# Kernel tuning notes

Measured on AMD Instinct MI355X. Metric: run time of the kernel, lower is better.

## Reference

```python
import jax, jax.numpy as jnp
import numpy as np

NUM_LABELS = 64
BATCH = 1024
SEQ_LEN = 512


def setup_inputs() -> dict:
    key = jax.random.key(0)
    k1, k2, k3, k4 = jax.random.split(key, 4)
    emissions = jax.random.normal(k1, (BATCH, SEQ_LEN, NUM_LABELS), dtype=jnp.float32)
    mask = jnp.ones((BATCH, SEQ_LEN), dtype=jnp.int32)
    # params: uniform(-0.1, 0.1) as in nn.init.uniform_
    transitions = jax.random.uniform(k2, (NUM_LABELS, NUM_LABELS), minval=-0.1, maxval=0.1, dtype=jnp.float32)
    start_transitions = jax.random.uniform(k3, (NUM_LABELS,), minval=-0.1, maxval=0.1, dtype=jnp.float32)
    end_transitions = jax.random.uniform(k4, (NUM_LABELS,), minval=-0.1, maxval=0.1, dtype=jnp.float32)
    return {
        "emissions": emissions,
        "mask": mask,
        "transitions": transitions,
        "start_transitions": start_transitions,
        "end_transitions": end_transitions,
    }


def reference(emissions, mask, transitions, start_transitions, end_transitions):
    """CRF forward algorithm (log partition) -> [batch]."""
    # initial alpha: start + emissions at t=0  -> [B, L]
    score0 = start_transitions + emissions[:, 0]

    # scan over time steps 1..S-1
    emit_rest = jnp.swapaxes(emissions[:, 1:], 0, 1)          # [S-1, B, L]
    mask_rest = jnp.swapaxes(mask[:, 1:], 0, 1)               # [S-1, B]

    def step(score, xs):
        emit_t, mask_t = xs                                   # [B, L], [B]
        # [B, L_prev, 1] + [L_prev, L_next] + [B, 1, L_next]
        next_score = jax.nn.logsumexp(
            score[:, :, None] + transitions[None] + emit_t[:, None, :], axis=1
        )                                                     # [B, L]
        score = jnp.where(mask_t[:, None].astype(bool), next_score, score)
        return score, None

    score, _ = jax.lax.scan(step, score0, (emit_rest, mask_rest))
    return jax.nn.logsumexp(score + end_transitions, axis=1)  # [B]
```

## Files before the change

kernel.cpp:

```cpp
#include <hip/hip_runtime.h>

#define NL 64
#define SQ 512
#define BATCH 1024
#define TMID 256

typedef __fp16 hf2 __attribute__((ext_vector_type(2)));

#define EXP2F(x)  __builtin_amdgcn_exp2f(x)
#define LOG2F(x)  __builtin_amdgcn_logf(x)

__device__ __forceinline__ float lane0_bcast(float v) {
    return __uint_as_float(__builtin_amdgcn_readfirstlane(__float_as_uint(v)));
}
__device__ __forceinline__ hf2 bc2(int pki, int lane) {
    int v = __builtin_amdgcn_readlane(pki, lane);
    return __builtin_bit_cast(hf2, v);
}

__global__ __launch_bounds__(64, 2) void crf_scan(
    const float* __restrict__ emissions,
    const int*   __restrict__ mask,
    const float* __restrict__ trans,
    const float* __restrict__ start_t,
    const float* __restrict__ end_t,
    float* __restrict__ ws_p,
    float* __restrict__ ws_c)
{
    const int  blk = blockIdx.x;
    const bool fwd = blk < BATCH;
    const int  b   = fwd ? blk : blk - BATCH;
    const int  j   = threadIdx.x;
    const float LOG2E = 1.44269504088896340736f;

    const float* em = emissions + (size_t)b * SQ * NL;
    const int*   mk = mask + (size_t)b * SQ;

    hf2 et2[NL / 2];
#pragma unroll
    for (int k = 0; k < NL / 2; ++k) {
        float e0, e1;
        if (fwd) { e0 = __expf(trans[(2*k + 0) * NL + j]);
                   e1 = __expf(trans[(2*k + 1) * NL + j]); }
        else     { e0 = __expf(trans[j * NL + (2*k + 0)]);
                   e1 = __expf(trans[j * NL + (2*k + 1)]); }
        et2[k] = __builtin_amdgcn_cvt_pkrtz(e0, e1);
    }

    auto matvec = [&](float xb) -> float {
        int nb = __builtin_amdgcn_update_dpp(0, __float_as_int(xb),
                                             0xB1, 0xF, 0xF, true);
        hf2 pk = __builtin_amdgcn_cvt_pkrtz(xb, __int_as_float(nb));
        int pki = __builtin_bit_cast(int, pk);
        float a0 = 0.f, a1 = 0.f, a2 = 0.f, a3 = 0.f;
#pragma unroll
        for (int k = 0; k < 32; k += 4) {
            a0 = __builtin_amdgcn_fdot2(bc2(pki, 2*(k+0)), et2[k+0], a0, false);
            a1 = __builtin_amdgcn_fdot2(bc2(pki, 2*(k+1)), et2[k+1], a1, false);
            a2 = __builtin_amdgcn_fdot2(bc2(pki, 2*(k+2)), et2[k+2], a2, false);
            a3 = __builtin_amdgcn_fdot2(bc2(pki, 2*(k+3)), et2[k+3], a3, false);
        }
        return (a0 + a1) + (a2 + a3);
    };

    float p, logC2;

    if (fwd) {
        const float s0f = start_t[j] + em[j];
        const float C   = lane0_bcast(s0f);
        p = EXP2F((s0f - C) * LOG2E);  logC2 = C * LOG2E;

        auto step = [&](float r, int m) {
            const float ex   = EXP2F(r * LOG2E);
            const float p0   = lane0_bcast(p);
            const float sinv = 0.25f * __builtin_amdgcn_rcpf(p0);
            const float mv   = matvec(p * sinv);
            if (m) { p = ex * mv; logC2 += LOG2F(p0) + 2.0f; }
        };

        float r0 = em[1*NL + j], r1 = em[2*NL + j];
        float r2 = em[3*NL + j], r3 = em[4*NL + j];

        for (int g = 0; g < 63; ++g) {
            const int t = 1 + 4 * g;
            const float e0 = r0, e1 = r1, e2 = r2, e3 = r3;
            int t7 = t + 7; if (t7 > TMID - 1) t7 = TMID - 1;
            r0 = em[(t+4)*NL + j]; r1 = em[(t+5)*NL + j];
            r2 = em[(t+6)*NL + j]; r3 = em[t7*NL + j];
            const int m0 = mk[t], m1 = mk[t+1], m2 = mk[t+2], m3 = mk[t+3];
            step(e0, m0); step(e1, m1); step(e2, m2); step(e3, m3);
        }
        step(r0, mk[253]); step(r1, mk[254]); step(r2, mk[255]);
    } else {
        p = __expf(end_t[j]);  logC2 = 0.f;

        auto step = [&](float r, int m) {
            const float ex   = EXP2F(r * LOG2E);
            const float sc   = ex * p;
            const float s0   = lane0_bcast(sc);
            const float sinv = 0.25f * __builtin_amdgcn_rcpf(s0);
            const float mv   = matvec(sc * sinv);
            if (m) { p = mv; logC2 += LOG2F(s0) + 2.0f; }
        };

        float r0 = em[511*NL + j], r1 = em[510*NL + j];
        float r2 = em[509*NL + j], r3 = em[508*NL + j];

        for (int g = 0; g < 64; ++g) {
            const int t = 511 - 4 * g;
            const float e0 = r0, e1 = r1, e2 = r2, e3 = r3;
            int t4 = t-4, t5 = t-5, t6 = t-6, t7 = t-7;
            if (t4 < TMID) t4 = TMID;  if (t5 < TMID) t5 = TMID;
            if (t6 < TMID) t6 = TMID;  if (t7 < TMID) t7 = TMID;
            r0 = em[t4*NL + j]; r1 = em[t5*NL + j];
            r2 = em[t6*NL + j]; r3 = em[t7*NL + j];
            const int m0 = mk[t], m1 = mk[t-1], m2 = mk[t-2], m3 = mk[t-3];
            step(e0, m0); step(e1, m1); step(e2, m2); step(e3, m3);
        }
    }

    ws_p[(size_t)blk * NL + j] = p;
    if (j == 0) ws_c[blk] = logC2;
}

__global__ __launch_bounds__(64) void crf_combine(
    const float* __restrict__ ws_p, const float* __restrict__ ws_c,
    float* __restrict__ out)
{
    const int b = blockIdx.x;
    const int j = threadIdx.x;
    float v = ws_p[(size_t)b * NL + j] * ws_p[(size_t)(b + BATCH) * NL + j];
#pragma unroll
    for (int off = 32; off; off >>= 1) v += __shfl_xor(v, off);
    if (j == 0)
        out[b] = 0.69314718055994530942f *
                 (ws_c[b] + ws_c[b + BATCH] + LOG2F(v));
}

extern "C" void kernel_launch(void* const* d_in, const int* in_sizes, int n_in,
                              void* d_out, int out_size, void* d_ws, size_t ws_size,
                              hipStream_t stream) {
    const float* emissions = (const float*)d_in[0];
    const int*   mask      = (const int*)d_in[1];
    const float* trans     = (const float*)d_in[2];
    const float* start_t   = (const float*)d_in[3];
    const float* end_t     = (const float*)d_in[4];
    float* out = (float*)d_out;

    float* ws_p = (float*)d_ws;
    float* ws_c = ws_p + 2 * BATCH * NL;

    crf_scan<<<2 * BATCH, NL, 0, stream>>>(emissions, mask, trans,
                                           start_t, end_t, ws_p, ws_c);
    crf_combine<<<BATCH, NL, 0, stream>>>(ws_p, ws_c, out);
}
```

Before: 249.1 us.

## Use exponent-bit power-of-two rescaling and deeper 8-step prefetch with vector mask loads

The per-step normalization no longer uses rcp and log2 on the lane-0 value. It reads that value's float exponent bits and scales by an exact power of two, accumulating integer exponents to shorten the serial dependency chain. The time loop is restructured into 8-step groups with one group of emissions prefetched ahead and masks loaded as int4 vectors, and the matvec uses 8 independent accumulators. The risk is a coarser normalization range (a factor of up to 2 instead of exact), which may affect fp16 precision in the packed dot products.

```diff
diff --git a/kernel.cpp b/kernel.cpp
--- a/kernel.cpp
+++ b/kernel.cpp
@@ -53,74 +53,121 @@
         hf2 pk = __builtin_amdgcn_cvt_pkrtz(xb, __int_as_float(nb));
         int pki = __builtin_bit_cast(int, pk);
         float a0 = 0.f, a1 = 0.f, a2 = 0.f, a3 = 0.f;
+        float a4 = 0.f, a5 = 0.f, a6 = 0.f, a7 = 0.f;
 #pragma unroll
-        for (int k = 0; k < 32; k += 4) {
+        for (int k = 0; k < 32; k += 8) {
             a0 = __builtin_amdgcn_fdot2(bc2(pki, 2*(k+0)), et2[k+0], a0, false);
             a1 = __builtin_amdgcn_fdot2(bc2(pki, 2*(k+1)), et2[k+1], a1, false);
             a2 = __builtin_amdgcn_fdot2(bc2(pki, 2*(k+2)), et2[k+2], a2, false);
             a3 = __builtin_amdgcn_fdot2(bc2(pki, 2*(k+3)), et2[k+3], a3, false);
+            a4 = __builtin_amdgcn_fdot2(bc2(pki, 2*(k+4)), et2[k+4], a4, false);
+            a5 = __builtin_amdgcn_fdot2(bc2(pki, 2*(k+5)), et2[k+5], a5, false);
+            a6 = __builtin_amdgcn_fdot2(bc2(pki, 2*(k+6)), et2[k+6], a6, false);
+            a7 = __builtin_amdgcn_fdot2(bc2(pki, 2*(k+7)), et2[k+7], a7, false);
         }
-        return (a0 + a1) + (a2 + a3);
+        return ((a0 + a1) + (a2 + a3)) + ((a4 + a5) + (a6 + a7));
     };
 
-    float p, logC2;
+    float p, base;
+    int   esum = 0;
 
     if (fwd) {
+        float pe1 = em[1*NL + j], pe2 = em[2*NL + j], pe3 = em[3*NL + j];
+        int   pm1 = mk[1], pm2 = mk[2], pm3 = mk[3];
+        float r0 = em[ 4*NL + j], r1 = em[ 5*NL + j];
+        float r2 = em[ 6*NL + j], r3 = em[ 7*NL + j];
+        float r4 = em[ 8*NL + j], r5 = em[ 9*NL + j];
+        float r6 = em[10*NL + j], r7 = em[11*NL + j];
+        int4 M0 = *reinterpret_cast<const int4*>(mk + 4);
+        int4 M1 = *reinterpret_cast<const int4*>(mk + 8);
+
         const float s0f = start_t[j] + em[j];
         const float C   = lane0_bcast(s0f);
-        p = EXP2F((s0f - C) * LOG2E);  logC2 = C * LOG2E;
+        p = EXP2F((s0f - C) * LOG2E);  base = C * LOG2E;
 
         auto step = [&](float r, int m) {
-            const float ex   = EXP2F(r * LOG2E);
-            const float p0   = lane0_bcast(p);
-            const float sinv = 0.25f * __builtin_amdgcn_rcpf(p0);
-            const float mv   = matvec(p * sinv);
-            if (m) { p = ex * mv; logC2 += LOG2F(p0) + 2.0f; }
+            const float ex = EXP2F(r * LOG2E);
+            const unsigned u = __builtin_amdgcn_readfirstlane(__float_as_uint(p));
+            const int eb = (int)((u >> 23) & 0xffu);
+            const float scale = __uint_as_float((unsigned)(251 - eb) << 23);
+            const float mv = matvec(p * scale);
+            if (m) { p = ex * mv; esum += eb - 124; }
         };
 
-        float r0 = em[1*NL + j], r1 = em[2*NL + j];
-        float r2 = em[3*NL + j], r3 = em[4*NL + j];
-
-        for (int g = 0; g < 63; ++g) {
-            const int t = 1 + 4 * g;
-            const float e0 = r0, e1 = r1, e2 = r2, e3 = r3;
-            int t7 = t + 7; if (t7 > TMID - 1) t7 = TMID - 1;
-            r0 = em[(t+4)*NL + j]; r1 = em[(t+5)*NL + j];
-            r2 = em[(t+6)*NL + j]; r3 = em[t7*NL + j];
-            const int m0 = mk[t], m1 = mk[t+1], m2 = mk[t+2], m3 = mk[t+3];
-            step(e0, m0); step(e1, m1); step(e2, m2); step(e3, m3);
+        step(pe1, pm1); step(pe2, pm2); step(pe3, pm3);
+
+        for (int G = 0; G < 31; ++G) {
+            const int t0 = 4 + 8 * G;
+            const int t8 = t0 + 8;
+            const int tA = (t0+12 > 255) ? 255 : t0+12;
+            const int tB = (t0+13 > 255) ? 255 : t0+13;
+            const int tC = (t0+14 > 255) ? 255 : t0+14;
+            const int tD = (t0+15 > 255) ? 255 : t0+15;
+            float n0 = em[(t8+0)*NL + j], n1 = em[(t8+1)*NL + j];
+            float n2 = em[(t8+2)*NL + j], n3 = em[(t8+3)*NL + j];
+            float n4 = em[tA*NL + j],     n5 = em[tB*NL + j];
+            float n6 = em[tC*NL + j],     n7 = em[tD*NL + j];
+            int4 nM0 = *reinterpret_cast<const int4*>(mk + t8);
+            const int tm1 = (t0+12 > 252) ? 252 : t0+12;
+            int4 nM1 = *reinterpret_cast<const int4*>(mk + tm1);
+
+            step(r0, M0.x); step(r1, M0.y); step(r2, M0.z); step(r3, M0.w);
+            step(r4, M1.x); step(r5, M1.y); step(r6, M1.z); step(r7, M1.w);
+
+            r0=n0; r1=n1; r2=n2; r3=n3; r4=n4; r5=n5; r6=n6; r7=n7;
+            M0=nM0; M1=nM1;
         }
-        step(r0, mk[253]); step(r1, mk[254]); step(r2, mk[255]);
+        step(r0, M0.x); step(r1, M0.y); step(r2, M0.z); step(r3, M0.w);
     } else {
-        p = __expf(end_t[j]);  logC2 = 0.f;
-
-        auto step = [&](float r, int m) {
-            const float ex   = EXP2F(r * LOG2E);
-            const float sc   = ex * p;
-            const float s0   = lane0_bcast(sc);
-            const float sinv = 0.25f * __builtin_amdgcn_rcpf(s0);
-            const float mv   = matvec(sc * sinv);
-            if (m) { p = mv; logC2 += LOG2F(s0) + 2.0f; }
-        };
-
         float r0 = em[511*NL + j], r1 = em[510*NL + j];
         float r2 = em[509*NL + j], r3 = em[508*NL + j];
-
-        for (int g = 0; g < 64; ++g) {
-            const int t = 511 - 4 * g;
-            const float e0 = r0, e1 = r1, e2 = r2, e3 = r3;
-            int t4 = t-4, t5 = t-5, t6 = t-6, t7 = t-7;
-            if (t4 < TMID) t4 = TMID;  if (t5 < TMID) t5 = TMID;
-            if (t6 < TMID) t6 = TMID;  if (t7 < TMID) t7 = TMID;
-            r0 = em[t4*NL + j]; r1 = em[t5*NL + j];
-            r2 = em[t6*NL + j]; r3 = em[t7*NL + j];
-            const int m0 = mk[t], m1 = mk[t-1], m2 = mk[t-2], m3 = mk[t-3];
-            step(e0, m0); step(e1, m1); step(e2, m2); step(e3, m3);
+        float r4 = em[507*NL + j], r5 = em[506*NL + j];
+        float r6 = em[505*NL + j], r7 = em[504*NL + j];
+        int4 Ma = *reinterpret_cast<const int4*>(mk + 508);
+        int4 Mb = *reinterpret_cast<const int4*>(mk + 504);
+
+        p = __expf(end_t[j]);  base = 0.f;
+
+        auto step = [&](float r, int m) {
+            const float ex = EXP2F(r * LOG2E);
+            const float sc = ex * p;
+            const unsigned u = __builtin_amdgcn_readfirstlane(__float_as_uint(sc));
+            const int eb = (int)((u >> 23) & 0xffu);
+            const float scale = __uint_as_float((unsigned)(251 - eb) << 23);
+            const float mv = matvec(sc * scale);
+            if (m) { p = mv; esum += eb - 124; }
+        };
+
+        for (int G = 0; G < 32; ++G) {
+            const int t0 = 511 - 8 * G;
+            const int tb = t0 - 8;
+            const int te0 = (tb-0 < 256) ? 256 : tb-0;
+            const int te1 = (tb-1 < 256) ? 256 : tb-1;
+            const int te2 = (tb-2 < 256) ? 256 : tb-2;
+            const int te3 = (tb-3 < 256) ? 256 : tb-3;
+            const int te4 = (tb-4 < 256) ? 256 : tb-4;
+            const int te5 = (tb-5 < 256) ? 256 : tb-5;
+            const int te6 = (tb-6 < 256) ? 256 : tb-6;
+            const int te7 = (tb-7 < 256) ? 256 : tb-7;
+            float n0 = em[te0*NL + j], n1 = em[te1*NL + j];
+            float n2 = em[te2*NL + j], n3 = em[te3*NL + j];
+            float n4 = em[te4*NL + j], n5 = em[te5*NL + j];
+            float n6 = em[te6*NL + j], n7 = em[te7*NL + j];
+            const int ta  = (tb-3 < 256) ? 256 : tb-3;
+            const int tbb = (tb-7 < 256) ? 256 : tb-7;
+            int4 nMa = *reinterpret_cast<const int4*>(mk + ta);
+            int4 nMb = *reinterpret_cast<const int4*>(mk + tbb);
+
+            step(r0, Ma.w); step(r1, Ma.z); step(r2, Ma.y); step(r3, Ma.x);
+            step(r4, Mb.w); step(r5, Mb.z); step(r6, Mb.y); step(r7, Mb.x);
+
+            r0=n0; r1=n1; r2=n2; r3=n3; r4=n4; r5=n5; r6=n6; r7=n7;
+            Ma=nMa; Mb=nMb;
         }
     }
 
     ws_p[(size_t)blk * NL + j] = p;
-    if (j == 0) ws_c[blk] = logC2;
+    if (j == 0) ws_c[blk] = base + (float)esum;
 }
 
 __global__ __launch_bounds__(64) void crf_combine(
```

New measurement: 245.9 us. No clear change (-1.3%).

## Interleave two batch chains per wavefront and use exponent-based power-of-two rescaling

Applied to the files above, without the earlier changes.

Each wavefront now runs the forward or backward recurrence for two batch elements at once. Their matvecs interleave, so the readlane/fdot2 dependency chains of one can hide the latency of the other, while the transition matrix in registers is shared between them. Per-step normalization no longer uses rcp and log2. It extracts the exponent bits of lane 0 and scales by an exact power of two, accumulating integer exponents. Emission prefetch is deepened to 8 steps and masks are loaded as int4. The grid halves to 1024 blocks with launch bounds of 1 wave per SIMD, which raises register pressure and leaves fewer waves in flight.

```diff
diff --git a/kernel.cpp b/kernel.cpp
--- a/kernel.cpp
+++ b/kernel.cpp
@@ -18,7 +18,7 @@
     return __builtin_bit_cast(hf2, v);
 }
 
-__global__ __launch_bounds__(64, 2) void crf_scan(
+__global__ __launch_bounds__(64, 1) void crf_scan(
     const float* __restrict__ emissions,
     const int*   __restrict__ mask,
     const float* __restrict__ trans,
@@ -28,13 +28,16 @@
     float* __restrict__ ws_c)
 {
     const int  blk = blockIdx.x;
-    const bool fwd = blk < BATCH;
-    const int  b   = fwd ? blk : blk - BATCH;
+    const bool fwd = blk < (BATCH / 2);
+    const int  bA  = fwd ? 2 * blk : 2 * (blk - BATCH / 2);
+    const int  bB  = bA + 1;
     const int  j   = threadIdx.x;
     const float LOG2E = 1.44269504088896340736f;
 
-    const float* em = emissions + (size_t)b * SQ * NL;
-    const int*   mk = mask + (size_t)b * SQ;
+    const float* emA = emissions + (size_t)bA * SQ * NL;
+    const float* emB = emissions + (size_t)bB * SQ * NL;
+    const int*   mkA = mask + (size_t)bA * SQ;
+    const int*   mkB = mask + (size_t)bB * SQ;
 
     hf2 et2[NL / 2];
 #pragma unroll
@@ -47,80 +50,207 @@
         et2[k] = __builtin_amdgcn_cvt_pkrtz(e0, e1);
     }
 
-    auto matvec = [&](float xb) -> float {
-        int nb = __builtin_amdgcn_update_dpp(0, __float_as_int(xb),
+    auto matvec2 = [&](float xA, float xB, float& oA, float& oB) {
+        int nA = __builtin_amdgcn_update_dpp(0, __float_as_int(xA),
                                              0xB1, 0xF, 0xF, true);
-        hf2 pk = __builtin_amdgcn_cvt_pkrtz(xb, __int_as_float(nb));
-        int pki = __builtin_bit_cast(int, pk);
+        int nB = __builtin_amdgcn_update_dpp(0, __float_as_int(xB),
+                                             0xB1, 0xF, 0xF, true);
+        hf2 pkA = __builtin_amdgcn_cvt_pkrtz(xA, __int_as_float(nA));
+        hf2 pkB = __builtin_amdgcn_cvt_pkrtz(xB, __int_as_float(nB));
+        int piA = __builtin_bit_cast(int, pkA);
+        int piB = __builtin_bit_cast(int, pkB);
         float a0 = 0.f, a1 = 0.f, a2 = 0.f, a3 = 0.f;
+        float b0 = 0.f, b1 = 0.f, b2 = 0.f, b3 = 0.f;
 #pragma unroll
         for (int k = 0; k < 32; k += 4) {
-            a0 = __builtin_amdgcn_fdot2(bc2(pki, 2*(k+0)), et2[k+0], a0, false);
-            a1 = __builtin_amdgcn_fdot2(bc2(pki, 2*(k+1)), et2[k+1], a1, false);
-            a2 = __builtin_amdgcn_fdot2(bc2(pki, 2*(k+2)), et2[k+2], a2, false);
-            a3 = __builtin_amdgcn_fdot2(bc2(pki, 2*(k+3)), et2[k+3], a3, false);
+            hf2 sA0 = bc2(piA, 2*(k+0)), sB0 = bc2(piB, 2*(k+0));
+            hf2 sA1 = bc2(piA, 2*(k+1)), sB1 = bc2(piB, 2*(k+1));
+            hf2 sA2 = bc2(piA, 2*(k+2)), sB2 = bc2(piB, 2*(k+2));
+            hf2 sA3 = bc2(piA, 2*(k+3)), sB3 = bc2(piB, 2*(k+3));
+            a0 = __builtin_amdgcn_fdot2(sA0, et2[k+0], a0, false);
+            b0 = __builtin_amdgcn_fdot2(sB0, et2[k+0], b0, false);
+            a1 = __builtin_amdgcn_fdot2(sA1, et2[k+1], a1, false);
+            b1 = __builtin_amdgcn_fdot2(sB1, et2[k+1], b1, false);
+            a2 = __builtin_amdgcn_fdot2(sA2, et2[k+2], a2, false);
+            b2 = __builtin_amdgcn_fdot2(sB2, et2[k+2], b2, false);
+            a3 = __builtin_amdgcn_fdot2(sA3, et2[k+3], a3, false);
+            b3 = __builtin_amdgcn_fdot2(sB3, et2[k+3], b3, false);
         }
-        return (a0 + a1) + (a2 + a3);
+        oA = (a0 + a1) + (a2 + a3);
+        oB = (b0 + b1) + (b2 + b3);
     };
 
-    float p, logC2;
+    float pA, pB, baseA, baseB;
+    int   esumA = 0, esumB = 0;
 
     if (fwd) {
-        const float s0f = start_t[j] + em[j];
-        const float C   = lane0_bcast(s0f);
-        p = EXP2F((s0f - C) * LOG2E);  logC2 = C * LOG2E;
-
-        auto step = [&](float r, int m) {
-            const float ex   = EXP2F(r * LOG2E);
-            const float p0   = lane0_bcast(p);
-            const float sinv = 0.25f * __builtin_amdgcn_rcpf(p0);
-            const float mv   = matvec(p * sinv);
-            if (m) { p = ex * mv; logC2 += LOG2F(p0) + 2.0f; }
+        auto stepPair = [&](float rA, int mA, float rB, int mB) {
+            const float exA = EXP2F(rA * LOG2E);
+            const float exB = EXP2F(rB * LOG2E);
+            const unsigned uA = __builtin_amdgcn_readfirstlane(__float_as_uint(pA));
+            const unsigned uB = __builtin_amdgcn_readfirstlane(__float_as_uint(pB));
+            const int ebA = (int)((uA >> 23) & 0xffu);
+            const int ebB = (int)((uB >> 23) & 0xffu);
+            const float scA = __uint_as_float((unsigned)(251 - ebA) << 23);
+            const float scB = __uint_as_float((unsigned)(251 - ebB) << 23);
+            float mvA, mvB;
+            matvec2(pA * scA, pB * scB, mvA, mvB);
+            if (mA) { pA = exA * mvA; esumA += ebA - 124; }
+            if (mB) { pB = exB * mvB; esumB += ebB - 124; }
         };
 
-        float r0 = em[1*NL + j], r1 = em[2*NL + j];
-        float r2 = em[3*NL + j], r3 = em[4*NL + j];
-
-        for (int g = 0; g < 63; ++g) {
-            const int t = 1 + 4 * g;
-            const float e0 = r0, e1 = r1, e2 = r2, e3 = r3;
-            int t7 = t + 7; if (t7 > TMID - 1) t7 = TMID - 1;
-            r0 = em[(t+4)*NL + j]; r1 = em[(t+5)*NL + j];
-            r2 = em[(t+6)*NL + j]; r3 = em[t7*NL + j];
-            const int m0 = mk[t], m1 = mk[t+1], m2 = mk[t+2], m3 = mk[t+3];
-            step(e0, m0); step(e1, m1); step(e2, m2); step(e3, m3);
+        const float s0A = start_t[j] + emA[j];
+        const float s0B = start_t[j] + emB[j];
+        const float CA = lane0_bcast(s0A), CB = lane0_bcast(s0B);
+        pA = EXP2F((s0A - CA) * LOG2E);  baseA = CA * LOG2E;
+        pB = EXP2F((s0B - CB) * LOG2E);  baseB = CB * LOG2E;
+
+        float peA1 = emA[1*NL + j], peA2 = emA[2*NL + j], peA3 = emA[3*NL + j];
+        float peB1 = emB[1*NL + j], peB2 = emB[2*NL + j], peB3 = emB[3*NL + j];
+        int pmA1 = mkA[1], pmA2 = mkA[2], pmA3 = mkA[3];
+        int pmB1 = mkB[1], pmB2 = mkB[2], pmB3 = mkB[3];
+        float rA0 = emA[ 4*NL + j], rA1 = emA[ 5*NL + j];
+        float rA2 = emA[ 6*NL + j], rA3 = emA[ 7*NL + j];
+        float rA4 = emA[ 8*NL + j], rA5 = emA[ 9*NL + j];
+        float rA6 = emA[10*NL + j], rA7 = emA[11*NL + j];
+        float rB0 = emB[ 4*NL + j], rB1 = emB[ 5*NL + j];
+        float rB2 = emB[ 6*NL + j], rB3 = emB[ 7*NL + j];
+        float rB4 = emB[ 8*NL + j], rB5 = emB[ 9*NL + j];
+        float rB6 = emB[10*NL + j], rB7 = emB[11*NL + j];
+        int4 MA0 = *reinterpret_cast<const int4*>(mkA + 4);
+        int4 MA1 = *reinterpret_cast<const int4*>(mkA + 8);
+        int4 MB0 = *reinterpret_cast<const int4*>(mkB + 4);
+        int4 MB1 = *reinterpret_cast<const int4*>(mkB + 8);
+
+        stepPair(peA1, pmA1, peB1, pmB1);
+        stepPair(peA2, pmA2, peB2, pmB2);
+        stepPair(peA3, pmA3, peB3, pmB3);
+
+        for (int G = 0; G < 31; ++G) {
+            const int t0 = 4 + 8 * G;
+            const int t8 = t0 + 8;
+            const int tA = (t0+12 > 255) ? 255 : t0+12;
+            const int tB = (t0+13 > 255) ? 255 : t0+13;
+            const int tC = (t0+14 > 255) ? 255 : t0+14;
+            const int tD = (t0+15 > 255) ? 255 : t0+15;
+            float nA0 = emA[(t8+0)*NL + j], nA1 = emA[(t8+1)*NL + j];
+            float nA2 = emA[(t8+2)*NL + j], nA3 = emA[(t8+3)*NL + j];
+            float nA4 = emA[tA*NL + j],     nA5 = emA[tB*NL + j];
+            float nA6 = emA[tC*NL + j],     nA7 = emA[tD*NL + j];
+            float nB0 = emB[(t8+0)*NL + j], nB1 = emB[(t8+1)*NL + j];
+            float nB2 = emB[(t8+2)*NL + j], nB3 = emB[(t8+3)*NL + j];
+            float nB4 = emB[tA*NL + j],     nB5 = emB[tB*NL + j];
+            float nB6 = emB[tC*NL + j],     nB7 = emB[tD*NL + j];
+            const int tm1 = (t0+12 > 252) ? 252 : t0+12;
+            int4 nMA0 = *reinterpret_cast<const int4*>(mkA + t8);
+            int4 nMA1 = *reinterpret_cast<const int4*>(mkA + tm1);
+            int4 nMB0 = *reinterpret_cast<const int4*>(mkB + t8);
+            int4 nMB1 = *reinterpret_cast<const int4*>(mkB + tm1);
+
+            stepPair(rA0, MA0.x, rB0, MB0.x);
+            stepPair(rA1, MA0.y, rB1, MB0.y);
+            stepPair(rA2, MA0.z, rB2, MB0.z);
+            stepPair(rA3, MA0.w, rB3, MB0.w);
+            stepPair(rA4, MA1.x, rB4, MB1.x);
+            stepPair(rA5, MA1.y, rB5, MB1.y);
+            stepPair(rA6, MA1.z, rB6, MB1.z);
+            stepPair(rA7, MA1.w, rB7, MB1.w);
+
+            rA0=nA0; rA1=nA1; rA2=nA2; rA3=nA3;
+            rA4=nA4; rA5=nA5; rA6=nA6; rA7=nA7;
+            rB0=nB0; rB1=nB1; rB2=nB2; rB3=nB3;
+            rB4=nB4; rB5=nB5; rB6=nB6; rB7=nB7;
+            MA0=nMA0; MA1=nMA1; MB0=nMB0; MB1=nMB1;
         }
-        step(r0, mk[253]); step(r1, mk[254]); step(r2, mk[255]);
+        stepPair(rA0, MA0.x, rB0, MB0.x);
+        stepPair(rA1, MA0.y, rB1, MB0.y);
+        stepPair(rA2, MA0.z, rB2, MB0.z);
+        stepPair(rA3, MA0.w, rB3, MB0.w);
     } else {
-        p = __expf(end_t[j]);  logC2 = 0.f;
-
-        auto step = [&](float r, int m) {
-            const float ex   = EXP2F(r * LOG2E);
-            const float sc   = ex * p;
-            const float s0   = lane0_bcast(sc);
-            const float sinv = 0.25f * __builtin_amdgcn_rcpf(s0);
-            const float mv   = matvec(sc * sinv);
-            if (m) { p = mv; logC2 += LOG2F(s0) + 2.0f; }
+        auto stepPair = [&](float rA, int mA, float rB, int mB) {
+            const float exA = EXP2F(rA * LOG2E);
+            const float exB = EXP2F(rB * LOG2E);
+            const float scAv = exA * pA;
+            const float scBv = exB * pB;
+            const unsigned uA = __builtin_amdgcn_readfirstlane(__float_as_uint(scAv));
+            const unsigned uB = __builtin_amdgcn_readfirstlane(__float_as_uint(scBv));
+            const int ebA = (int)((uA >> 23) & 0xffu);
+            const int ebB = (int)((uB >> 23) & 0xffu);
+            const float scA = __uint_as_float((unsigned)(251 - ebA) << 23);
+            const float scB = __uint_as_float((unsigned)(251 - ebB) << 23);
+            float mvA, mvB;
+            matvec2(scAv * scA, scBv * scB, mvA, mvB);
+            if (mA) { pA = mvA; esumA += ebA - 124; }
+            if (mB) { pB = mvB; esumB += ebB - 124; }
         };
 
-        float r0 = em[511*NL + j], r1 = em[510*NL + j];
-        float r2 = em[509*NL + j], r3 = em[508*NL + j];
-
-        for (int g = 0; g < 64; ++g) {
-            const int t = 511 - 4 * g;
-            const float e0 = r0, e1 = r1, e2 = r2, e3 = r3;
-            int t4 = t-4, t5 = t-5, t6 = t-6, t7 = t-7;
-            if (t4 < TMID) t4 = TMID;  if (t5 < TMID) t5 = TMID;
-            if (t6 < TMID) t6 = TMID;  if (t7 < TMID) t7 = TMID;
-            r0 = em[t4*NL + j]; r1 = em[t5*NL + j];
-            r2 = em[t6*NL + j]; r3 = em[t7*NL + j];
-            const int m0 = mk[t], m1 = mk[t-1], m2 = mk[t-2], m3 = mk[t-3];
-            step(e0, m0); step(e1, m1); step(e2, m2); step(e3, m3);
+        float rA0 = emA[511*NL + j], rA1 = emA[510*NL + j];
+        float rA2 = emA[509*NL + j], rA3 = emA[508*NL + j];
+        float rA4 = emA[507*NL + j], rA5 = emA[506*NL + j];
+        float rA6 = emA[505*NL + j], rA7 = emA[504*NL + j];
+        float rB0 = emB[511*NL + j], rB1 = emB[510*NL + j];
+        float rB2 = emB[509*NL + j], rB3 = emB[508*NL + j];
+        float rB4 = emB[507*NL + j], rB5 = emB[506*NL + j];
+        float rB6 = emB[505*NL + j], rB7 = emB[504*NL + j];
+        int4 MAa = *reinterpret_cast<const int4*>(mkA + 508);
+        int4 MAb = *reinterpret_cast<const int4*>(mkA + 504);
+        int4 MBa = *reinterpret_cast<const int4*>(mkB + 508);
+        int4 MBb = *reinterpret_cast<const int4*>(mkB + 504);
+
+        pA = __expf(end_t[j]);  baseA = 0.f;
+        pB = pA;                baseB = 0.f;
+
+        for (int G = 0; G < 32; ++G) {
+            const int t0 = 511 - 8 * G;
+            const int tb = t0 - 8;
+            const int te0 = (tb-0 < 256) ? 256 : tb-0;
+            const int te1 = (tb-1 < 256) ? 256 : tb-1;
+            const int te2 = (tb-2 < 256) ? 256 : tb-2;
+            const int te3 = (tb-3 < 256) ? 256 : tb-3;
+            const int te4 = (tb-4 < 256) ? 256 : tb-4;
+            const int te5 = (tb-5 < 256) ? 256 : tb-5;
+            const int te6 = (tb-6 < 256) ? 256 : tb-6;
+            const int te7 = (tb-7 < 256) ? 256 : tb-7;
+            float nA0 = emA[te0*NL + j], nA1 = emA[te1*NL + j];
+            float nA2 = emA[te2*NL + j], nA3 = emA[te3*NL + j];
+            float nA4 = emA[te4*NL + j], nA5 = emA[te5*NL + j];
+            float nA6 = emA[te6*NL + j], nA7 = emA[te7*NL + j];
+            float nB0 = emB[te0*NL + j], nB1 = emB[te1*NL + j];
+            float nB2 = emB[te2*NL + j], nB3 = emB[te3*NL + j];
+            float nB4 = emB[te4*NL + j], nB5 = emB[te5*NL + j];
+            float nB6 = emB[te6*NL + j], nB7 = emB[te7*NL + j];
+            const int ta  = (tb-3 < 256) ? 256 : tb-3;
+            const int tbb = (tb-7 < 256) ? 256 : tb-7;
+            int4 nMAa = *reinterpret_cast<const int4*>(mkA + ta);
+            int4 nMAb = *reinterpret_cast<const int4*>(mkA + tbb);
+            int4 nMBa = *reinterpret_cast<const int4*>(mkB + ta);
+            int4 nMBb = *reinterpret_cast<const int4*>(mkB + tbb);
+
+            stepPair(rA0, MAa.w, rB0, MBa.w);
+            stepPair(rA1, MAa.z, rB1, MBa.z);
+            stepPair(rA2, MAa.y, rB2, MBa.y);
+            stepPair(rA3, MAa.x, rB3, MBa.x);
+            stepPair(rA4, MAb.w, rB4, MBb.w);
+            stepPair(rA5, MAb.z, rB5, MBb.z);
+            stepPair(rA6, MAb.y, rB6, MBb.y);
+            stepPair(rA7, MAb.x, rB7, MBb.x);
+
+            rA0=nA0; rA1=nA1; rA2=nA2; rA3=nA3;
+            rA4=nA4; rA5=nA5; rA6=nA6; rA7=nA7;
+            rB0=nB0; rB1=nB1; rB2=nB2; rB3=nB3;
+            rB4=nB4; rB5=nB5; rB6=nB6; rB7=nB7;
+            MAa=nMAa; MAb=nMAb; MBa=nMBa; MBb=nMBb;
         }
     }
 
-    ws_p[(size_t)blk * NL + j] = p;
-    if (j == 0) ws_c[blk] = logC2;
+    const int slotA = fwd ? bA : (BATCH + bA);
+    const int slotB = slotA + 1;
+    ws_p[(size_t)slotA * NL + j] = pA;
+    ws_p[(size_t)slotB * NL + j] = pB;
+    if (j == 0) {
+        ws_c[slotA] = baseA + (float)esumA;
+        ws_c[slotB] = baseB + (float)esumB;
+    }
 }
 
 __global__ __launch_bounds__(64) void crf_combine(
@@ -150,7 +280,7 @@
     float* ws_p = (float*)d_ws;
     float* ws_c = ws_p + 2 * BATCH * NL;
 
-    crf_scan<<<2 * BATCH, NL, 0, stream>>>(emissions, mask, trans,
-                                           start_t, end_t, ws_p, ws_c);
+    crf_scan<<<BATCH, NL, 0, stream>>>(emissions, mask, trans,
+                                       start_t, end_t, ws_p, ws_c);
     crf_combine<<<BATCH, NL, 0, stream>>>(ws_p, ws_c, out);
 }
```

Measured after the change: 254.7 us. 2.3% more time.

## Batch 16 CRF chains per wave and compute transitions matvec with MFMA

Applied to the files above, without the earlier changes.

Replaces the per-chain readlane/fdot2 matrix-vector product with 16x16x32 f16 MFMA instructions that process 16 sequences per wavefront, shrinking the grid from 2048 to 128 blocks. Normalisation switches from reciprocal/log to power-of-two exponent rescaling accumulated as an integer. Emissions are loaded as float4 vectors and prefetched one group ahead. This cuts instruction count per chain-step, at the cost of far fewer waves on the device and the added latency of dependent MFMA chains.

```diff
diff --git a/kernel.cpp b/kernel.cpp
--- a/kernel.cpp
+++ b/kernel.cpp
@@ -3,22 +3,21 @@
 #define NL 64
 #define SQ 512
 #define BATCH 1024
-#define TMID 256
-
-typedef __fp16 hf2 __attribute__((ext_vector_type(2)));
+
+typedef __fp16   hf2   __attribute__((ext_vector_type(2)));
+typedef _Float16 h8    __attribute__((ext_vector_type(8)));
+typedef float    f32x4 __attribute__((ext_vector_type(4)));
+typedef int      i32x4 __attribute__((ext_vector_type(4)));
 
 #define EXP2F(x)  __builtin_amdgcn_exp2f(x)
 #define LOG2F(x)  __builtin_amdgcn_logf(x)
-
-__device__ __forceinline__ float lane0_bcast(float v) {
-    return __uint_as_float(__builtin_amdgcn_readfirstlane(__float_as_uint(v)));
-}
-__device__ __forceinline__ hf2 bc2(int pki, int lane) {
-    int v = __builtin_amdgcn_readlane(pki, lane);
-    return __builtin_bit_cast(hf2, v);
-}
-
-__global__ __launch_bounds__(64, 2) void crf_scan(
+#define MFMA16(a,b,c) __builtin_amdgcn_mfma_f32_16x16x32_f16((a),(b),(c),0,0,0)
+
+static __device__ __forceinline__ int pkf16(float a, float b) {
+    return __builtin_bit_cast(int, __builtin_amdgcn_cvt_pkrtz(a, b));
+}
+
+__global__ __launch_bounds__(64, 1) void crf_scan_mfma(
     const float* __restrict__ emissions,
     const int*   __restrict__ mask,
     const float* __restrict__ trans,
@@ -27,100 +26,207 @@
     float* __restrict__ ws_p,
     float* __restrict__ ws_c)
 {
-    const int  blk = blockIdx.x;
-    const bool fwd = blk < BATCH;
-    const int  b   = fwd ? blk : blk - BATCH;
-    const int  j   = threadIdx.x;
+    const int  blk  = blockIdx.x;
+    const bool fwd  = blk < 64;
+    const int  cbase = (fwd ? blk : blk - 64) * 16;
+    const int  l  = threadIdx.x;
+    const int  cl = l & 15;
+    const int  g  = l >> 4;
+    const int  chain = cbase + cl;
     const float LOG2E = 1.44269504088896340736f;
 
-    const float* em = emissions + (size_t)b * SQ * NL;
-    const int*   mk = mask + (size_t)b * SQ;
-
-    hf2 et2[NL / 2];
-#pragma unroll
-    for (int k = 0; k < NL / 2; ++k) {
-        float e0, e1;
-        if (fwd) { e0 = __expf(trans[(2*k + 0) * NL + j]);
-                   e1 = __expf(trans[(2*k + 1) * NL + j]); }
-        else     { e0 = __expf(trans[j * NL + (2*k + 0)]);
-                   e1 = __expf(trans[j * NL + (2*k + 1)]); }
-        et2[k] = __builtin_amdgcn_cvt_pkrtz(e0, e1);
+    const float* em = emissions + (size_t)chain * SQ * NL;
+    const int*   mk = mask + (size_t)chain * SQ;
+    const int    bpa = cl * 4;
+
+    h8 Afr[4][2];
+#pragma unroll
+    for (int m = 0; m < 4; ++m) {
+#pragma unroll
+        for (int ks = 0; ks < 2; ++ks) {
+            i32x4 w;
+#pragma unroll
+            for (int ep = 0; ep < 4; ++ep) {
+                const int e0 = 2*ep, e1 = 2*ep + 1;
+                const int k0 = 32*ks + 16*(e0>>2) + 4*g + (e0&3);
+                const int k1 = 32*ks + 16*(e1>>2) + 4*g + (e1&3);
+                float v0, v1;
+                if (fwd) { v0 = __expf(trans[k0*NL + (16*m + cl)]);
+                           v1 = __expf(trans[k1*NL + (16*m + cl)]); }
+                else     { v0 = __expf(trans[(16*m + cl)*NL + k0]);
+                           v1 = __expf(trans[(16*m + cl)*NL + k1]); }
+                w[ep] = pkf16(v0, v1);
+            }
+            Afr[m][ks] = __builtin_bit_cast(h8, w);
+        }
     }
 
-    auto matvec = [&](float xb) -> float {
-        int nb = __builtin_amdgcn_update_dpp(0, __float_as_int(xb),
-                                             0xB1, 0xF, 0xF, true);
-        hf2 pk = __builtin_amdgcn_cvt_pkrtz(xb, __int_as_float(nb));
-        int pki = __builtin_bit_cast(int, pk);
-        float a0 = 0.f, a1 = 0.f, a2 = 0.f, a3 = 0.f;
-#pragma unroll
-        for (int k = 0; k < 32; k += 4) {
-            a0 = __builtin_amdgcn_fdot2(bc2(pki, 2*(k+0)), et2[k+0], a0, false);
-            a1 = __builtin_amdgcn_fdot2(bc2(pki, 2*(k+1)), et2[k+1], a1, false);
-            a2 = __builtin_amdgcn_fdot2(bc2(pki, 2*(k+2)), et2[k+2], a2, false);
-            a3 = __builtin_amdgcn_fdot2(bc2(pki, 2*(k+3)), et2[k+3], a3, false);
-        }
-        return (a0 + a1) + (a2 + a3);
+    const f32x4 zz = {0.f, 0.f, 0.f, 0.f};
+    f32x4 pD[4];
+    float basec = 0.f;
+    int   esum  = 0;
+
+    auto stepF = [&](const f32x4 (&E)[4], int mm) {
+        f32x4 ex[4];
+#pragma unroll
+        for (int m = 0; m < 4; ++m)
+#pragma unroll
+            for (int r = 0; r < 4; ++r) ex[m][r] = EXP2F(E[m][r] * LOG2E);
+        const int anci = __builtin_amdgcn_ds_bpermute(bpa, __float_as_int(pD[0][0]));
+        const unsigned u = (unsigned)anci;
+        const int eb = (int)((u >> 23) & 0xffu);
+        const float sc = __uint_as_float((unsigned)(251 - eb) << 23);
+        i32x4 w0, w1;
+        w0[0] = pkf16(pD[0][0]*sc, pD[0][1]*sc); w0[1] = pkf16(pD[0][2]*sc, pD[0][3]*sc);
+        w0[2] = pkf16(pD[1][0]*sc, pD[1][1]*sc); w0[3] = pkf16(pD[1][2]*sc, pD[1][3]*sc);
+        w1[0] = pkf16(pD[2][0]*sc, pD[2][1]*sc); w1[1] = pkf16(pD[2][2]*sc, pD[2][3]*sc);
+        w1[2] = pkf16(pD[3][0]*sc, pD[3][1]*sc); w1[3] = pkf16(pD[3][2]*sc, pD[3][3]*sc);
+        const h8 B0 = __builtin_bit_cast(h8, w0);
+        const h8 B1 = __builtin_bit_cast(h8, w1);
+        f32x4 ac[4];
+#pragma unroll
+        for (int m = 0; m < 4; ++m) {
+            ac[m] = MFMA16(Afr[m][0], B0, zz);
+            ac[m] = MFMA16(Afr[m][1], B1, ac[m]);
+        }
+#pragma unroll
+        for (int m = 0; m < 4; ++m)
+#pragma unroll
+            for (int r = 0; r < 4; ++r)
+                pD[m][r] = mm ? (ex[m][r] * ac[m][r]) : pD[m][r];
+        esum += mm ? (eb - 124) : 0;
     };
 
-    float p, logC2;
+    auto stepB = [&](const f32x4 (&E)[4], int mm) {
+        f32x4 scv[4];
+#pragma unroll
+        for (int m = 0; m < 4; ++m)
+#pragma unroll
+            for (int r = 0; r < 4; ++r)
+                scv[m][r] = EXP2F(E[m][r] * LOG2E) * pD[m][r];
+        const int anci = __builtin_amdgcn_ds_bpermute(bpa, __float_as_int(scv[0][0]));
+        const unsigned u = (unsigned)anci;
+        const int eb = (int)((u >> 23) & 0xffu);
+        const float sc = __uint_as_float((unsigned)(251 - eb) << 23);
+        i32x4 w0, w1;
+        w0[0] = pkf16(scv[0][0]*sc, scv[0][1]*sc); w0[1] = pkf16(scv[0][2]*sc, scv[0][3]*sc);
+        w0[2] = pkf16(scv[1][0]*sc, scv[1][1]*sc); w0[3] = pkf16(scv[1][2]*sc, scv[1][3]*sc);
+        w1[0] = pkf16(scv[2][0]*sc, scv[2][1]*sc); w1[1] = pkf16(scv[2][2]*sc, scv[2][3]*sc);
+        w1[2] = pkf16(scv[3][0]*sc, scv[3][1]*sc); w1[3] = pkf16(scv[3][2]*sc, scv[3][3]*sc);
+        const h8 B0 = __builtin_bit_cast(h8, w0);
+        const h8 B1 = __builtin_bit_cast(h8, w1);
+        f32x4 ac[4];
+#pragma unroll
+        for (int m = 0; m < 4; ++m) {
+            ac[m] = MFMA16(Afr[m][0], B0, zz);
+            ac[m] = MFMA16(Afr[m][1], B1, ac[m]);
+        }
+#pragma unroll
+        for (int m = 0; m < 4; ++m)
+#pragma unroll
+            for (int r = 0; r < 4; ++r)
+                pD[m][r] = mm ? ac[m][r] : pD[m][r];
+        esum += mm ? (eb - 124) : 0;
+    };
 
     if (fwd) {
-        const float s0f = start_t[j] + em[j];
-        const float C   = lane0_bcast(s0f);
-        p = EXP2F((s0f - C) * LOG2E);  logC2 = C * LOG2E;
-
-        auto step = [&](float r, int m) {
-            const float ex   = EXP2F(r * LOG2E);
-            const float p0   = lane0_bcast(p);
-            const float sinv = 0.25f * __builtin_amdgcn_rcpf(p0);
-            const float mv   = matvec(p * sinv);
-            if (m) { p = ex * mv; logC2 += LOG2F(p0) + 2.0f; }
-        };
-
-        float r0 = em[1*NL + j], r1 = em[2*NL + j];
-        float r2 = em[3*NL + j], r3 = em[4*NL + j];
-
-        for (int g = 0; g < 63; ++g) {
-            const int t = 1 + 4 * g;
-            const float e0 = r0, e1 = r1, e2 = r2, e3 = r3;
-            int t7 = t + 7; if (t7 > TMID - 1) t7 = TMID - 1;
-            r0 = em[(t+4)*NL + j]; r1 = em[(t+5)*NL + j];
-            r2 = em[(t+6)*NL + j]; r3 = em[t7*NL + j];
-            const int m0 = mk[t], m1 = mk[t+1], m2 = mk[t+2], m3 = mk[t+3];
-            step(e0, m0); step(e1, m1); step(e2, m2); step(e3, m3);
-        }
-        step(r0, mk[253]); step(r1, mk[254]); step(r2, mk[255]);
+        f32x4 s0[4];
+#pragma unroll
+        for (int m = 0; m < 4; ++m) {
+            const f32x4 st = *reinterpret_cast<const f32x4*>(start_t + 16*m + 4*g);
+            const f32x4 e0 = *reinterpret_cast<const f32x4*>(em + 16*m + 4*g);
+            s0[m] = st + e0;
+        }
+        const int anci = __builtin_amdgcn_ds_bpermute(bpa, __float_as_int(s0[0][0]));
+        const float anc = __int_as_float(anci);
+        basec = anc * LOG2E;
+#pragma unroll
+        for (int m = 0; m < 4; ++m)
+#pragma unroll
+            for (int r = 0; r < 4; ++r)
+                pD[m][r] = EXP2F((s0[m][r] - anc) * LOG2E);
+
+        f32x4 P[3][4];
+#pragma unroll
+        for (int k = 0; k < 3; ++k)
+#pragma unroll
+            for (int m = 0; m < 4; ++m)
+                P[k][m] = *reinterpret_cast<const f32x4*>(em + (size_t)(1+k)*NL + 16*m + 4*g);
+        const i32x4 M0 = *reinterpret_cast<const i32x4*>(mk);
+
+        f32x4 C[4][4];
+#pragma unroll
+        for (int k = 0; k < 4; ++k)
+#pragma unroll
+            for (int m = 0; m < 4; ++m)
+                C[k][m] = *reinterpret_cast<const f32x4*>(em + (size_t)(4+k)*NL + 16*m + 4*g);
+        i32x4 Mc = *reinterpret_cast<const i32x4*>(mk + 4);
+
+        stepF(P[0], M0[1]); stepF(P[1], M0[2]); stepF(P[2], M0[3]);
+
+        for (int G = 0; G < 63; ++G) {
+            const int t = 4 + 4*G;
+            f32x4 Nb[4][4];
+#pragma unroll
+            for (int k = 0; k < 4; ++k)
+#pragma unroll
+                for (int m = 0; m < 4; ++m)
+                    Nb[k][m] = *reinterpret_cast<const f32x4*>(em + (size_t)(t+4+k)*NL + 16*m + 4*g);
+            const i32x4 Mn = *reinterpret_cast<const i32x4*>(mk + t + 4);
+
+            stepF(C[0], Mc[0]); stepF(C[1], Mc[1]);
+            stepF(C[2], Mc[2]); stepF(C[3], Mc[3]);
+
+#pragma unroll
+            for (int k = 0; k < 4; ++k)
+#pragma unroll
+                for (int m = 0; m < 4; ++m) C[k][m] = Nb[k][m];
+            Mc = Mn;
+        }
     } else {
-        p = __expf(end_t[j]);  logC2 = 0.f;
-
-        auto step = [&](float r, int m) {
-            const float ex   = EXP2F(r * LOG2E);
-            const float sc   = ex * p;
-            const float s0   = lane0_bcast(sc);
-            const float sinv = 0.25f * __builtin_amdgcn_rcpf(s0);
-            const float mv   = matvec(sc * sinv);
-            if (m) { p = mv; logC2 += LOG2F(s0) + 2.0f; }
-        };
-
-        float r0 = em[511*NL + j], r1 = em[510*NL + j];
-        float r2 = em[509*NL + j], r3 = em[508*NL + j];
-
-        for (int g = 0; g < 64; ++g) {
-            const int t = 511 - 4 * g;
-            const float e0 = r0, e1 = r1, e2 = r2, e3 = r3;
-            int t4 = t-4, t5 = t-5, t6 = t-6, t7 = t-7;
-            if (t4 < TMID) t4 = TMID;  if (t5 < TMID) t5 = TMID;
-            if (t6 < TMID) t6 = TMID;  if (t7 < TMID) t7 = TMID;
-            r0 = em[t4*NL + j]; r1 = em[t5*NL + j];
-            r2 = em[t6*NL + j]; r3 = em[t7*NL + j];
-            const int m0 = mk[t], m1 = mk[t-1], m2 = mk[t-2], m3 = mk[t-3];
-            step(e0, m0); step(e1, m1); step(e2, m2); step(e3, m3);
+#pragma unroll
+        for (int m = 0; m < 4; ++m) {
+            const f32x4 ev = *reinterpret_cast<const f32x4*>(end_t + 16*m + 4*g);
+#pragma unroll
+            for (int r = 0; r < 4; ++r) pD[m][r] = __expf(ev[r]);
+        }
+        basec = 0.f;
+
+        f32x4 C[4][4];
+#pragma unroll
+        for (int k = 0; k < 4; ++k)
+#pragma unroll
+            for (int m = 0; m < 4; ++m)
+                C[k][m] = *reinterpret_cast<const f32x4*>(em + (size_t)(511-k)*NL + 16*m + 4*g);
+        i32x4 Mc = *reinterpret_cast<const i32x4*>(mk + 508);
+
+        for (int G = 0; G < 64; ++G) {
+            const int t0 = 511 - 4*G;
+            const int tp = t0 - 4;
+            f32x4 Nb[4][4];
+#pragma unroll
+            for (int k = 0; k < 4; ++k)
+#pragma unroll
+                for (int m = 0; m < 4; ++m)
+                    Nb[k][m] = *reinterpret_cast<const f32x4*>(em + (size_t)(tp-k)*NL + 16*m + 4*g);
+            const i32x4 Mn = *reinterpret_cast<const i32x4*>(mk + (tp - 3));
+
+            stepB(C[0], Mc[3]); stepB(C[1], Mc[2]);
+            stepB(C[2], Mc[1]); stepB(C[3], Mc[0]);
+
+#pragma unroll
+            for (int k = 0; k < 4; ++k)
+#pragma unroll
+                for (int m = 0; m < 4; ++m) C[k][m] = Nb[k][m];
+            Mc = Mn;
         }
     }
 
-    ws_p[(size_t)blk * NL + j] = p;
-    if (j == 0) ws_c[blk] = logC2;
+    const int slot = (fwd ? 0 : BATCH) + chain;
+#pragma unroll
+    for (int m = 0; m < 4; ++m)
+        *reinterpret_cast<f32x4*>(ws_p + (size_t)slot*NL + 16*m + 4*g) = pD[m];
+    if (g == 0) ws_c[slot] = basec + (float)esum;
 }
 
 __global__ __launch_bounds__(64) void crf_combine(
@@ -150,7 +256,7 @@
     float* ws_p = (float*)d_ws;
     float* ws_c = ws_p + 2 * BATCH * NL;
 
-    crf_scan<<<2 * BATCH, NL, 0, stream>>>(emissions, mask, trans,
-                                           start_t, end_t, ws_p, ws_c);
+    crf_scan_mfma<<<128, NL, 0, stream>>>(emissions, mask, trans,
+                                          start_t, end_t, ws_p, ws_c);
     crf_combine<<<BATCH, NL, 0, stream>>>(ws_p, ws_c, out);
 }
```

After: 290.3 us. +16.5%, slower.
